# Optimization experiments

Measured on AMD Instinct MI355X. Metric: run time of the kernel, lower is better.

The kernel has to match this reference:

```python
import jax, jax.numpy as jnp
import numpy as np

N = 50000       # nodes
E = 1_600_000   # edges (before self-loops)
IN = 128        # in_channels
OUT = 32        # out_channels per head
H = 2           # heads
NEG_SLOPE = 0.2 # PyG GATConv default leaky-relu slope


def setup_inputs() -> dict:
    key = jax.random.key(0)
    k = jax.random.split(key, 6)
    x = jax.random.normal(k[0], (N, IN), jnp.float32)
    edge_index = jax.random.randint(k[1], (2, E), 0, N, dtype=jnp.int64)
    W = jax.random.normal(k[2], (IN, H * OUT), jnp.float32) / np.sqrt(IN).astype(np.float32)
    att_src = jax.random.normal(k[3], (H, OUT), jnp.float32) * 0.1
    att_dst = jax.random.normal(k[4], (H, OUT), jnp.float32) * 0.1
    bias = jax.random.normal(k[5], (H * OUT,), jnp.float32) * 0.01
    return {"x": x, "edge_index": edge_index, "W": W,
            "att_src": att_src, "att_dst": att_dst, "bias": bias}


def reference(x, edge_index, W, att_src, att_dst, bias):
    n = x.shape[0]
    h_, c = att_src.shape
    # add self-loops (PyG GATConv default add_self_loops=True)
    loops = jnp.arange(n, dtype=edge_index.dtype)
    src = jnp.concatenate([edge_index[0], loops])  # [E+N]
    dst = jnp.concatenate([edge_index[1], loops])  # [E+N]
    # linear transform -> [N, H, C]
    h = (x @ W).reshape(n, h_, c)
    # per-node attention logits per head
    a_src = jnp.einsum('nhc,hc->nh', h, att_src)  # [N, H]
    a_dst = jnp.einsum('nhc,hc->nh', h, att_dst)  # [N, H]
    # per-edge scores
    e = jax.nn.leaky_relu(a_src[src] + a_dst[dst], NEG_SLOPE)  # [E+N, H]
    # segment softmax over incoming edges of each dst node
    seg_max = jax.ops.segment_max(e, dst, num_segments=n)      # [N, H]
    ex = jnp.exp(e - seg_max[dst])
    denom = jax.ops.segment_sum(ex, dst, num_segments=n)       # [N, H]
    alpha = ex / denom[dst]                                    # [E+N, H]
    # weighted scatter-aggregate of source features
    msg = alpha[:, :, None] * h[src]                           # [E+N, H, C]
    out = jax.ops.segment_sum(msg, dst, num_segments=n)        # [N, H, C]
    return out.reshape(n, h_ * c) + bias
```

## Files before the change

kernel.cpp:

```cpp
#include <hip/hip_runtime.h>
#include <hip/hip_fp16.h>

#define N_NODES 50000
#define N_EDGES 1600000
#define IN_CH   128
#define NEG     0.2f
#define NBUK    391
#define BCAP    4608
#define CAP     80
#define CHUNK   4096
#define P_BLOCKS 391
#define PT      512

static __device__ __forceinline__ __half2 u2h2(unsigned u) {
    union { unsigned u; __half2 h; } x; x.u = u; return x.h;
}

__global__ __launch_bounds__(256) void gemm_logits(
    const float* __restrict__ x, const float* __restrict__ W,
    const float* __restrict__ att_src, const float* __restrict__ att_dst,
    unsigned int* __restrict__ hI, float* __restrict__ as_, float* __restrict__ ad_,
    int* __restrict__ gcur)
{
    if (blockIdx.x == 0) {
        for (int i = threadIdx.x; i < NBUK; i += 256) gcur[i] = 0;
    }

    __shared__ float Wl[IN_CH * 64];
    for (int i = threadIdx.x; i < IN_CH * 64; i += 256) Wl[i] = W[i];
    __syncthreads();

    int gid = blockIdx.x * 256 + threadIdx.x;
    int row = gid >> 2;
    int sub = gid & 3;
    if (row >= N_NODES) return;

    float acc[16];
#pragma unroll
    for (int c = 0; c < 16; ++c) acc[c] = 0.f;

    const float* xr = x + (size_t)row * IN_CH;
    for (int k = 0; k < IN_CH; k += 4) {
        float4 xv = *(const float4*)(xr + k);
        float xs[4] = {xv.x, xv.y, xv.z, xv.w};
#pragma unroll
        for (int kk = 0; kk < 4; ++kk) {
            const float* wr = &Wl[(k + kk) * 64 + sub * 16];
#pragma unroll
            for (int c = 0; c < 16; c += 4) {
                float4 wv = *(const float4*)(wr + c);
                acc[c]     += xs[kk] * wv.x;
                acc[c + 1] += xs[kk] * wv.y;
                acc[c + 2] += xs[kk] * wv.z;
                acc[c + 3] += xs[kk] * wv.w;
            }
        }
    }

    float part[16];
#pragma unroll
    for (int i = 0; i < 16; ++i) part[i] = __shfl_xor(acc[i], 2);

    if (sub < 2) {
        union { unsigned int u[16]; uint4 v4[4]; } pk;
#pragma unroll
        for (int i = 0; i < 16; ++i) {
            pk.u[i] = (unsigned)__half_as_ushort(__float2half_rn(acc[i])) |
                      ((unsigned)__half_as_ushort(__float2half_rn(part[i])) << 16);
        }
        uint4* hp = (uint4*)(hI + (size_t)row * 32 + sub * 16);
#pragma unroll
        for (int i = 0; i < 4; ++i) hp[i] = pk.v4[i];
    }

    float s = 0.f, d = 0.f;
#pragma unroll
    for (int c = 0; c < 16; ++c) {
        s += acc[c] * att_src[sub * 16 + c];
        d += acc[c] * att_dst[sub * 16 + c];
    }
    s += __shfl_xor(s, 1);
    d += __shfl_xor(d, 1);
    if ((sub & 1) == 0) {
        as_[row * 2 + (sub >> 1)] = s;
        ad_[row * 2 + (sub >> 1)] = d;
    }
}

__global__ __launch_bounds__(PT) void partition(
    const int* __restrict__ ei, int* __restrict__ gcur,
    unsigned int* __restrict__ barr)
{
    __shared__ int hist[NBUK];
    __shared__ int start[NBUK];
    __shared__ int gbase[NBUK];
    __shared__ int lofs[NBUK];
    __shared__ int wsum[8];
    __shared__ int woff[8];
    __shared__ unsigned int buf[CHUNK];

    int tid = threadIdx.x;
    int lane = tid & 63, wid = tid >> 6;
    int cbase = blockIdx.x * CHUNK;
    int cnt = N_EDGES - cbase;
    if (cnt > CHUNK) cnt = CHUNK;
    int n4 = cnt >> 2;

    for (int i = tid; i < NBUK; i += PT) { hist[i] = 0; lofs[i] = 0; }
    __syncthreads();

    const int4* s4 = (const int4*)ei + (cbase >> 2);
    const int4* d4 = (const int4*)(ei + N_EDGES) + (cbase >> 2);

    int4 dv[2], sv[2];
#pragma unroll
    for (int i = 0; i < 2; ++i) {
        int k = i * PT + tid;
        if (k < n4) {
            dv[i] = d4[k]; sv[i] = s4[k];
            atomicAdd(&hist[dv[i].x >> 7], 1);
            atomicAdd(&hist[dv[i].y >> 7], 1);
            atomicAdd(&hist[dv[i].z >> 7], 1);
            atomicAdd(&hist[dv[i].w >> 7], 1);
        }
    }
    __syncthreads();

    int a = (tid < NBUK) ? hist[tid] : 0;
    int orig = a;
#pragma unroll
    for (int off = 1; off < 64; off <<= 1) {
        int u = __shfl_up(a, off);
        if (lane >= off) a += u;
    }
    if (lane == 63) wsum[wid] = a;
    __syncthreads();
    if (tid == 0) {
        int r = 0;
#pragma unroll
        for (int w = 0; w < 8; ++w) { woff[w] = r; r += wsum[w]; }
    }
    __syncthreads();
    a += woff[wid];
    if (tid < NBUK) {
        start[tid] = a - orig;
        gbase[tid] = atomicAdd(&gcur[tid], orig);
    }
    __syncthreads();

#pragma unroll
    for (int i = 0; i < 2; ++i) {
        int k = i * PT + tid;
        if (k < n4) {
            int dd[4] = {dv[i].x, dv[i].y, dv[i].z, dv[i].w};
            int ss[4] = {sv[i].x, sv[i].y, sv[i].z, sv[i].w};
#pragma unroll
            for (int e = 0; e < 4; ++e) {
                int d = dd[e];
                int bkt = d >> 7;
                int loc = atomicAdd(&lofs[bkt], 1);
                buf[start[bkt] + loc] =
                    (unsigned)ss[e] | ((unsigned)(d & 127) << 16) | ((unsigned)bkt << 23);
            }
        }
    }
    __syncthreads();

    for (int i = tid; i < cnt; i += PT) {
        unsigned u = buf[i];
        int bkt = u >> 23;
        int g = gbase[bkt] + (i - start[bkt]);
        if (g < BCAP) barr[(size_t)bkt * BCAP + g] = u & 0x7FFFFFu;
    }
}

__global__ __launch_bounds__(512) void aggregate(
    const unsigned int* __restrict__ hI, const float* __restrict__ as_,
    const float* __restrict__ ad_, const int* __restrict__ gcur,
    const unsigned int* __restrict__ barr, const float* __restrict__ bias,
    float* __restrict__ out)
{
    __shared__ unsigned short lcol[32 * CAP];
    __shared__ int hist[32];

    int b     = blockIdx.x >> 2;
    int jbase = (blockIdx.x & 3) << 5;
    int tid   = threadIdx.x;
    if (tid < 32) hist[tid] = 0;
    __syncthreads();

    int cnt = gcur[b];
    if (cnt > BCAP) cnt = BCAP;
    const unsigned int* bb = barr + (size_t)b * BCAP;

    for (int i = tid; i < cnt; i += 512) {
        unsigned u = bb[i];
        int r = ((int)(u >> 16) & 127) - jbase;
        if ((unsigned)r < 32u) {
            int k = atomicAdd(&hist[r], 1);
            if (k < CAP) lcol[r * CAP + k] = (unsigned short)(u & 0xFFFFu);
        }
    }
    __syncthreads();

    int lane = tid & 63;
    int wave = tid >> 6;
    int c    = lane & 31;
    int hv   = lane >> 5;
    int sl   = lane & 32;
    float bi0 = bias[c], bi1 = bias[32 + c];

    for (int pass = 0; pass < 2; ++pass) {
        int r = pass * 16 + (wave << 1) + hv;
        int node = b * 128 + jbase + r;
        bool valid = (node < N_NODES);

        float2 adv = valid ? *(const float2*)(ad_ + node * 2) : make_float2(0.f, 0.f);
        float2 asv = valid ? *(const float2*)(as_ + node * 2) : make_float2(0.f, 0.f);

        float t0 = asv.x + adv.x, t1 = asv.y + adv.y;
        float e0 = (t0 > 0.f) ? t0 : NEG * t0;
        float e1 = (t1 > 0.f) ? t1 : NEG * t1;
        float p0s = __expf(e0), p1s = __expf(e1);
        unsigned hs = valid ? hI[(unsigned)node * 32u + c] : 0u;
        __half2 hsh = u2h2(hs);
        float self0 = p0s * __half2float(__low2half(hsh));
        float self1 = p1s * __half2float(__high2half(hsh));
        float s0 = 0.f, s1 = 0.f;

        __half2 z = __float2half2_rn(0.f);
        __half2 acA = z, acB = z, acC = z, acD = z;

        int n = valid ? min(hist[r], CAP) : 0;
        const unsigned short* cb = &lcol[r * CAP];
        int nmax = max(n, __shfl_xor(n, 32));

        for (int base = 0; base < nmax; base += 32) {
            unsigned msrc = 0, packP = 0;
            int myidx = base + c;
            if (myidx < n) {
                int srci = (int)cb[myidx];
                float2 av = *(const float2*)(as_ + srci * 2);
                float u0 = av.x + adv.x, u1 = av.y + adv.y;
                float f0 = (u0 > 0.f) ? u0 : NEG * u0;
                float f1 = (u1 > 0.f) ? u1 : NEG * u1;
                float q0 = __expf(f0), q1 = __expf(f1);
                s0 += q0; s1 += q1;
                msrc  = (unsigned)srci;
                packP = (unsigned)__half_as_ushort(__float2half_rn(q0)) |
                        ((unsigned)__half_as_ushort(__float2half_rn(q1)) << 16);
            }
            int c32 = nmax - base;
            if (c32 > 32) c32 = 32;

            int jj = 0;
            for (; jj + 8 <= c32; jj += 8) {
                unsigned sA = __shfl(msrc, sl + jj);
                unsigned sB = __shfl(msrc, sl + jj + 1);
                unsigned sC = __shfl(msrc, sl + jj + 2);
                unsigned sD = __shfl(msrc, sl + jj + 3);
                unsigned sE = __shfl(msrc, sl + jj + 4);
                unsigned sF = __shfl(msrc, sl + jj + 5);
                unsigned sG = __shfl(msrc, sl + jj + 6);
                unsigned sH = __shfl(msrc, sl + jj + 7);
                unsigned pA = __shfl(packP, sl + jj);
                unsigned pB = __shfl(packP, sl + jj + 1);
                unsigned pC = __shfl(packP, sl + jj + 2);
                unsigned pD = __shfl(packP, sl + jj + 3);
                unsigned pE = __shfl(packP, sl + jj + 4);
                unsigned pF = __shfl(packP, sl + jj + 5);
                unsigned pG = __shfl(packP, sl + jj + 6);
                unsigned pH = __shfl(packP, sl + jj + 7);
                unsigned vA = hI[sA * 32u + c];
                unsigned vB = hI[sB * 32u + c];
                unsigned vC = hI[sC * 32u + c];
                unsigned vD = hI[sD * 32u + c];
                unsigned vE = hI[sE * 32u + c];
                unsigned vF = hI[sF * 32u + c];
                unsigned vG = hI[sG * 32u + c];
                unsigned vH = hI[sH * 32u + c];
                acA = __hfma2(u2h2(vA), u2h2(pA), acA);
                acB = __hfma2(u2h2(vB), u2h2(pB), acB);
                acC = __hfma2(u2h2(vC), u2h2(pC), acC);
                acD = __hfma2(u2h2(vD), u2h2(pD), acD);
                acA = __hfma2(u2h2(vE), u2h2(pE), acA);
                acB = __hfma2(u2h2(vF), u2h2(pF), acB);
                acC = __hfma2(u2h2(vG), u2h2(pG), acC);
                acD = __hfma2(u2h2(vH), u2h2(pH), acD);
            }
            for (; jj < c32; ++jj) {
                unsigned sA = __shfl(msrc, sl + jj);
                unsigned pA = __shfl(packP, sl + jj);
                unsigned vA = hI[sA * 32u + c];
                acA = __hfma2(u2h2(vA), u2h2(pA), acA);
            }
        }

        float2 fA = __half22float2(acA);
        float2 fB = __half22float2(acB);
        float2 fC = __half22float2(acC);
        float2 fD = __half22float2(acD);
        float acc0 = (fA.x + fB.x) + (fC.x + fD.x) + self0;
        float acc1 = (fA.y + fB.y) + (fC.y + fD.y) + self1;

        s0 += __shfl_xor(s0, 16); s1 += __shfl_xor(s1, 16);
        s0 += __shfl_xor(s0, 8);  s1 += __shfl_xor(s1, 8);
        s0 += __shfl_xor(s0, 4);  s1 += __shfl_xor(s1, 4);
        s0 += __shfl_xor(s0, 2);  s1 += __shfl_xor(s1, 2);
        s0 += __shfl_xor(s0, 1);  s1 += __shfl_xor(s1, 1);
        s0 += p0s; s1 += p1s;

        if (valid) {
            out[(size_t)node * 64 + c]      = acc0 / s0 + bi0;
            out[(size_t)node * 64 + 32 + c] = acc1 / s1 + bi1;
        }
    }
}

extern "C" void kernel_launch(void* const* d_in, const int* in_sizes, int n_in,
                              void* d_out, int out_size, void* d_ws, size_t ws_size,
                              hipStream_t stream)
{
    const float* x       = (const float*)d_in[0];
    const int*   ei      = (const int*)d_in[1];
    const float* W       = (const float*)d_in[2];
    const float* att_src = (const float*)d_in[3];
    const float* att_dst = (const float*)d_in[4];
    const float* bias    = (const float*)d_in[5];
    float* out = (float*)d_out;

    char* ws = (char*)d_ws;
    size_t off = 0;
    auto alloc = [&](size_t bytes) -> void* {
        void* p = ws + off;
        off = (off + bytes + 511) & ~(size_t)511;
        return p;
    };
    unsigned int* hI  = (unsigned int*)alloc((size_t)N_NODES * 32 * 4);
    float*  as_ = (float*)alloc((size_t)N_NODES * 2 * 4);
    float*  ad_ = (float*)alloc((size_t)N_NODES * 2 * 4);
    int*    gcur = (int*)alloc((size_t)NBUK * 4);
    unsigned int* barr = (unsigned int*)alloc((size_t)NBUK * BCAP * 4);

    gemm_logits<<<(N_NODES * 4 + 255) / 256, 256, 0, stream>>>(
        x, W, att_src, att_dst, hI, as_, ad_, gcur);
    partition<<<P_BLOCKS, PT, 0, stream>>>(ei, gcur, barr);
    aggregate<<<NBUK * 4, 512, 0, stream>>>(hI, as_, ad_, gcur, barr, bias, out);
}
```

Before: 81.45 us.

## Fuse GEMM and edge partition into one launch; batch 64 edges per aggregate iteration

The node-feature GEMM and the edge bucketing are merged into one kernel whose block ranges split between the two independent jobs. They now run concurrently and share a union of shared memory. Zeroing of the bucket counters moves to a tiny separate kernel. The aggregate loop now loads two 32-edge groups of source indices and logits up front before gathering, to expose more memory-level parallelism. The cost is an extra tiny launch, larger shared memory per block (which may limit occupancy), and more registers in the aggregate loop.

```diff
diff --git a/kernel.cpp b/kernel.cpp
--- a/kernel.cpp
+++ b/kernel.cpp
@@ -10,167 +10,167 @@
 #define CAP     80
 #define CHUNK   4096
 #define P_BLOCKS 391
-#define PT      512
+#define G_BLOCKS 391
 
 static __device__ __forceinline__ __half2 u2h2(unsigned u) {
     union { unsigned u; __half2 h; } x; x.u = u; return x.h;
 }
 
-__global__ __launch_bounds__(256) void gemm_logits(
+__global__ void zero_gcur(int* __restrict__ gcur)
+{
+    if (threadIdx.x < NBUK) gcur[threadIdx.x] = 0;
+}
+
+__global__ __launch_bounds__(512, 6) void fused_gp(
+    const int* __restrict__ ei, int* __restrict__ gcur,
+    unsigned int* __restrict__ barr,
     const float* __restrict__ x, const float* __restrict__ W,
     const float* __restrict__ att_src, const float* __restrict__ att_dst,
-    unsigned int* __restrict__ hI, float* __restrict__ as_, float* __restrict__ ad_,
-    int* __restrict__ gcur)
+    unsigned int* __restrict__ hI, float* __restrict__ as_, float* __restrict__ ad_)
 {
-    if (blockIdx.x == 0) {
-        for (int i = threadIdx.x; i < NBUK; i += 256) gcur[i] = 0;
-    }
-
-    __shared__ float Wl[IN_CH * 64];
-    for (int i = threadIdx.x; i < IN_CH * 64; i += 256) Wl[i] = W[i];
-    __syncthreads();
-
-    int gid = blockIdx.x * 256 + threadIdx.x;
-    int row = gid >> 2;
-    int sub = gid & 3;
-    if (row >= N_NODES) return;
-
-    float acc[16];
-#pragma unroll
-    for (int c = 0; c < 16; ++c) acc[c] = 0.f;
-
-    const float* xr = x + (size_t)row * IN_CH;
-    for (int k = 0; k < IN_CH; k += 4) {
-        float4 xv = *(const float4*)(xr + k);
-        float xs[4] = {xv.x, xv.y, xv.z, xv.w};
-#pragma unroll
-        for (int kk = 0; kk < 4; ++kk) {
-            const float* wr = &Wl[(k + kk) * 64 + sub * 16];
-#pragma unroll
-            for (int c = 0; c < 16; c += 4) {
-                float4 wv = *(const float4*)(wr + c);
-                acc[c]     += xs[kk] * wv.x;
-                acc[c + 1] += xs[kk] * wv.y;
-                acc[c + 2] += xs[kk] * wv.z;
-                acc[c + 3] += xs[kk] * wv.w;
-            }
-        }
-    }
-
-    float part[16];
-#pragma unroll
-    for (int i = 0; i < 16; ++i) part[i] = __shfl_xor(acc[i], 2);
-
-    if (sub < 2) {
-        union { unsigned int u[16]; uint4 v4[4]; } pk;
-#pragma unroll
-        for (int i = 0; i < 16; ++i) {
-            pk.u[i] = (unsigned)__half_as_ushort(__float2half_rn(acc[i])) |
-                      ((unsigned)__half_as_ushort(__float2half_rn(part[i])) << 16);
-        }
-        uint4* hp = (uint4*)(hI + (size_t)row * 32 + sub * 16);
-#pragma unroll
-        for (int i = 0; i < 4; ++i) hp[i] = pk.v4[i];
-    }
-
-    float s = 0.f, d = 0.f;
-#pragma unroll
-    for (int c = 0; c < 16; ++c) {
-        s += acc[c] * att_src[sub * 16 + c];
-        d += acc[c] * att_dst[sub * 16 + c];
-    }
-    s += __shfl_xor(s, 1);
-    d += __shfl_xor(d, 1);
-    if ((sub & 1) == 0) {
-        as_[row * 2 + (sub >> 1)] = s;
-        ad_[row * 2 + (sub >> 1)] = d;
-    }
-}
-
-__global__ __launch_bounds__(PT) void partition(
-    const int* __restrict__ ei, int* __restrict__ gcur,
-    unsigned int* __restrict__ barr)
-{
-    __shared__ int hist[NBUK];
-    __shared__ int start[NBUK];
-    __shared__ int gbase[NBUK];
-    __shared__ int lofs[NBUK];
-    __shared__ int wsum[8];
-    __shared__ int woff[8];
-    __shared__ unsigned int buf[CHUNK];
+    __shared__ union {
+        struct {
+            int hist[NBUK], start[NBUK], gbase[NBUK], lofs[NBUK];
+            int wsum[8], woff[8];
+            unsigned int buf[CHUNK];
+        } p;
+        float w[IN_CH * 64];
+    } sm;
 
     int tid = threadIdx.x;
-    int lane = tid & 63, wid = tid >> 6;
-    int cbase = blockIdx.x * CHUNK;
-    int cnt = N_EDGES - cbase;
-    if (cnt > CHUNK) cnt = CHUNK;
-    int n4 = cnt >> 2;
-
-    for (int i = tid; i < NBUK; i += PT) { hist[i] = 0; lofs[i] = 0; }
-    __syncthreads();
-
-    const int4* s4 = (const int4*)ei + (cbase >> 2);
-    const int4* d4 = (const int4*)(ei + N_EDGES) + (cbase >> 2);
-
-    int4 dv[2], sv[2];
-#pragma unroll
-    for (int i = 0; i < 2; ++i) {
-        int k = i * PT + tid;
-        if (k < n4) {
-            dv[i] = d4[k]; sv[i] = s4[k];
-            atomicAdd(&hist[dv[i].x >> 7], 1);
-            atomicAdd(&hist[dv[i].y >> 7], 1);
-            atomicAdd(&hist[dv[i].z >> 7], 1);
-            atomicAdd(&hist[dv[i].w >> 7], 1);
-        }
-    }
-    __syncthreads();
-
-    int a = (tid < NBUK) ? hist[tid] : 0;
-    int orig = a;
-#pragma unroll
-    for (int off = 1; off < 64; off <<= 1) {
-        int u = __shfl_up(a, off);
-        if (lane >= off) a += u;
-    }
-    if (lane == 63) wsum[wid] = a;
-    __syncthreads();
-    if (tid == 0) {
-        int r = 0;
-#pragma unroll
-        for (int w = 0; w < 8; ++w) { woff[w] = r; r += wsum[w]; }
-    }
-    __syncthreads();
-    a += woff[wid];
-    if (tid < NBUK) {
-        start[tid] = a - orig;
-        gbase[tid] = atomicAdd(&gcur[tid], orig);
-    }
-    __syncthreads();
-
-#pragma unroll
-    for (int i = 0; i < 2; ++i) {
-        int k = i * PT + tid;
-        if (k < n4) {
-            int dd[4] = {dv[i].x, dv[i].y, dv[i].z, dv[i].w};
-            int ss[4] = {sv[i].x, sv[i].y, sv[i].z, sv[i].w};
-#pragma unroll
-            for (int e = 0; e < 4; ++e) {
-                int d = dd[e];
-                int bkt = d >> 7;
-                int loc = atomicAdd(&lofs[bkt], 1);
-                buf[start[bkt] + loc] =
-                    (unsigned)ss[e] | ((unsigned)(d & 127) << 16) | ((unsigned)bkt << 23);
-            }
-        }
-    }
-    __syncthreads();
-
-    for (int i = tid; i < cnt; i += PT) {
-        unsigned u = buf[i];
-        int bkt = u >> 23;
-        int g = gbase[bkt] + (i - start[bkt]);
-        if (g < BCAP) barr[(size_t)bkt * BCAP + g] = u & 0x7FFFFFu;
+
+    if (blockIdx.x < P_BLOCKS) {
+        int lane = tid & 63, wid = tid >> 6;
+        int cbase = blockIdx.x * CHUNK;
+        int cnt = N_EDGES - cbase;
+        if (cnt > CHUNK) cnt = CHUNK;
+        int n4 = cnt >> 2;
+
+        for (int i = tid; i < NBUK; i += 512) { sm.p.hist[i] = 0; sm.p.lofs[i] = 0; }
+        __syncthreads();
+
+        const int4* s4 = (const int4*)ei + (cbase >> 2);
+        const int4* d4 = (const int4*)(ei + N_EDGES) + (cbase >> 2);
+
+        int4 dv[2], sv[2];
+#pragma unroll
+        for (int i = 0; i < 2; ++i) {
+            int k = i * 512 + tid;
+            if (k < n4) {
+                dv[i] = d4[k]; sv[i] = s4[k];
+                atomicAdd(&sm.p.hist[dv[i].x >> 7], 1);
+                atomicAdd(&sm.p.hist[dv[i].y >> 7], 1);
+                atomicAdd(&sm.p.hist[dv[i].z >> 7], 1);
+                atomicAdd(&sm.p.hist[dv[i].w >> 7], 1);
+            }
+        }
+        __syncthreads();
+
+        int a = (tid < NBUK) ? sm.p.hist[tid] : 0;
+        int orig = a;
+#pragma unroll
+        for (int off = 1; off < 64; off <<= 1) {
+            int u = __shfl_up(a, off);
+            if (lane >= off) a += u;
+        }
+        if (lane == 63) sm.p.wsum[wid] = a;
+        __syncthreads();
+        if (tid == 0) {
+            int r = 0;
+#pragma unroll
+            for (int w = 0; w < 8; ++w) { sm.p.woff[w] = r; r += sm.p.wsum[w]; }
+        }
+        __syncthreads();
+        a += sm.p.woff[wid];
+        if (tid < NBUK) {
+            sm.p.start[tid] = a - orig;
+            sm.p.gbase[tid] = atomicAdd(&gcur[tid], orig);
+        }
+        __syncthreads();
+
+#pragma unroll
+        for (int i = 0; i < 2; ++i) {
+            int k = i * 512 + tid;
+            if (k < n4) {
+                int dd[4] = {dv[i].x, dv[i].y, dv[i].z, dv[i].w};
+                int ss[4] = {sv[i].x, sv[i].y, sv[i].z, sv[i].w};
+#pragma unroll
+                for (int e = 0; e < 4; ++e) {
+                    int d = dd[e];
+                    int bkt = d >> 7;
+                    int loc = atomicAdd(&sm.p.lofs[bkt], 1);
+                    sm.p.buf[sm.p.start[bkt] + loc] =
+                        (unsigned)ss[e] | ((unsigned)(d & 127) << 16) | ((unsigned)bkt << 23);
+                }
+            }
+        }
+        __syncthreads();
+
+        for (int i = tid; i < cnt; i += 512) {
+            unsigned u = sm.p.buf[i];
+            int bkt = u >> 23;
+            int g = sm.p.gbase[bkt] + (i - sm.p.start[bkt]);
+            if (g < BCAP) barr[(size_t)bkt * BCAP + g] = u & 0x7FFFFFu;
+        }
+    } else {
+        for (int i = tid; i < IN_CH * 64; i += 512) sm.w[i] = W[i];
+        __syncthreads();
+
+        int gid = (blockIdx.x - P_BLOCKS) * 512 + tid;
+        int row = gid >> 2;
+        int sub = gid & 3;
+        if (row >= N_NODES) return;
+
+        float acc[16];
+#pragma unroll
+        for (int c = 0; c < 16; ++c) acc[c] = 0.f;
+
+        const float* xr = x + (size_t)row * IN_CH;
+        for (int k = 0; k < IN_CH; k += 4) {
+            float4 xv = *(const float4*)(xr + k);
+            float xs[4] = {xv.x, xv.y, xv.z, xv.w};
+#pragma unroll
+            for (int kk = 0; kk < 4; ++kk) {
+                const float* wr = &sm.w[(k + kk) * 64 + sub * 16];
+#pragma unroll
+                for (int c = 0; c < 16; c += 4) {
+                    float4 wv = *(const float4*)(wr + c);
+                    acc[c]     += xs[kk] * wv.x;
+                    acc[c + 1] += xs[kk] * wv.y;
+                    acc[c + 2] += xs[kk] * wv.z;
+                    acc[c + 3] += xs[kk] * wv.w;
+                }
+            }
+        }
+
+        float part[16];
+#pragma unroll
+        for (int i = 0; i < 16; ++i) part[i] = __shfl_xor(acc[i], 2);
+
+        if (sub < 2) {
+            union { unsigned int u[16]; uint4 v4[4]; } pk;
+#pragma unroll
+            for (int i = 0; i < 16; ++i) {
+                pk.u[i] = (unsigned)__half_as_ushort(__float2half_rn(acc[i])) |
+                          ((unsigned)__half_as_ushort(__float2half_rn(part[i])) << 16);
+            }
+            uint4* hp = (uint4*)(hI + (size_t)row * 32 + sub * 16);
+#pragma unroll
+            for (int i = 0; i < 4; ++i) hp[i] = pk.v4[i];
+        }
+
+        float s = 0.f, d = 0.f;
+#pragma unroll
+        for (int c = 0; c < 16; ++c) {
+            s += acc[c] * att_src[sub * 16 + c];
+            d += acc[c] * att_dst[sub * 16 + c];
+        }
+        s += __shfl_xor(s, 1);
+        d += __shfl_xor(d, 1);
+        if ((sub & 1) == 0) {
+            as_[row * 2 + (sub >> 1)] = s;
+            ad_[row * 2 + (sub >> 1)] = d;
+        }
     }
 }
 
@@ -235,42 +235,56 @@
         const unsigned short* cb = &lcol[r * CAP];
         int nmax = max(n, __shfl_xor(n, 32));
 
-        for (int base = 0; base < nmax; base += 32) {
-            unsigned msrc = 0, packP = 0;
-            int myidx = base + c;
-            if (myidx < n) {
-                int srci = (int)cb[myidx];
-                float2 av = *(const float2*)(as_ + srci * 2);
-                float u0 = av.x + adv.x, u1 = av.y + adv.y;
+        for (int base = 0; base < nmax; base += 64) {
+            unsigned ms0 = 0, pp0 = 0, ms1 = 0, pp1 = 0;
+            int i0 = base + c, i1 = base + 32 + c;
+            int sA_ = (i0 < n) ? (int)cb[i0] : -1;
+            int sB_ = (i1 < n) ? (int)cb[i1] : -1;
+            float2 avA = (sA_ >= 0) ? *(const float2*)(as_ + sA_ * 2) : make_float2(0.f, 0.f);
+            float2 avB = (sB_ >= 0) ? *(const float2*)(as_ + sB_ * 2) : make_float2(0.f, 0.f);
+            if (sA_ >= 0) {
+                float u0 = avA.x + adv.x, u1 = avA.y + adv.y;
                 float f0 = (u0 > 0.f) ? u0 : NEG * u0;
                 float f1 = (u1 > 0.f) ? u1 : NEG * u1;
                 float q0 = __expf(f0), q1 = __expf(f1);
                 s0 += q0; s1 += q1;
-                msrc  = (unsigned)srci;
-                packP = (unsigned)__half_as_ushort(__float2half_rn(q0)) |
-                        ((unsigned)__half_as_ushort(__float2half_rn(q1)) << 16);
-            }
-            int c32 = nmax - base;
-            if (c32 > 32) c32 = 32;
+                ms0 = (unsigned)sA_;
+                pp0 = (unsigned)__half_as_ushort(__float2half_rn(q0)) |
+                      ((unsigned)__half_as_ushort(__float2half_rn(q1)) << 16);
+            }
+            if (sB_ >= 0) {
+                float u0 = avB.x + adv.x, u1 = avB.y + adv.y;
+                float f0 = (u0 > 0.f) ? u0 : NEG * u0;
+                float f1 = (u1 > 0.f) ? u1 : NEG * u1;
+                float q0 = __expf(f0), q1 = __expf(f1);
+                s0 += q0; s1 += q1;
+                ms1 = (unsigned)sB_;
+                pp1 = (unsigned)__half_as_ushort(__float2half_rn(q0)) |
+                      ((unsigned)__half_as_ushort(__float2half_rn(q1)) << 16);
+            }
+
+            int rem = nmax - base;
+            int cA = rem < 32 ? rem : 32;
+            int cB = rem - 32; if (cB < 0) cB = 0; else if (cB > 32) cB = 32;
 
             int jj = 0;
-            for (; jj + 8 <= c32; jj += 8) {
-                unsigned sA = __shfl(msrc, sl + jj);
-                unsigned sB = __shfl(msrc, sl + jj + 1);
-                unsigned sC = __shfl(msrc, sl + jj + 2);
-                unsigned sD = __shfl(msrc, sl + jj + 3);
-                unsigned sE = __shfl(msrc, sl + jj + 4);
-                unsigned sF = __shfl(msrc, sl + jj + 5);
-                unsigned sG = __shfl(msrc, sl + jj + 6);
-                unsigned sH = __shfl(msrc, sl + jj + 7);
-                unsigned pA = __shfl(packP, sl + jj);
-                unsigned pB = __shfl(packP, sl + jj + 1);
-                unsigned pC = __shfl(packP, sl + jj + 2);
-                unsigned pD = __shfl(packP, sl + jj + 3);
-                unsigned pE = __shfl(packP, sl + jj + 4);
-                unsigned pF = __shfl(packP, sl + jj + 5);
-                unsigned pG = __shfl(packP, sl + jj + 6);
-                unsigned pH = __shfl(packP, sl + jj + 7);
+            for (; jj + 8 <= cA; jj += 8) {
+                unsigned sA = __shfl(ms0, sl + jj);
+                unsigned sB = __shfl(ms0, sl + jj + 1);
+                unsigned sC = __shfl(ms0, sl + jj + 2);
+                unsigned sD = __shfl(ms0, sl + jj + 3);
+                unsigned sE = __shfl(ms0, sl + jj + 4);
+                unsigned sF = __shfl(ms0, sl + jj + 5);
+                unsigned sG = __shfl(ms0, sl + jj + 6);
+                unsigned sH = __shfl(ms0, sl + jj + 7);
+                unsigned pA = __shfl(pp0, sl + jj);
+                unsigned pB = __shfl(pp0, sl + jj + 1);
+                unsigned pC = __shfl(pp0, sl + jj + 2);
+                unsigned pD = __shfl(pp0, sl + jj + 3);
+                unsigned pE = __shfl(pp0, sl + jj + 4);
+                unsigned pF = __shfl(pp0, sl + jj + 5);
+                unsigned pG = __shfl(pp0, sl + jj + 6);
+                unsigned pH = __shfl(pp0, sl + jj + 7);
                 unsigned vA = hI[sA * 32u + c];
                 unsigned vB = hI[sB * 32u + c];
                 unsigned vC = hI[sC * 32u + c];
@@ -288,9 +302,50 @@
                 acC = __hfma2(u2h2(vG), u2h2(pG), acC);
                 acD = __hfma2(u2h2(vH), u2h2(pH), acD);
             }
-            for (; jj < c32; ++jj) {
-                unsigned sA = __shfl(msrc, sl + jj);
-                unsigned pA = __shfl(packP, sl + jj);
+            for (; jj < cA; ++jj) {
+                unsigned sA = __shfl(ms0, sl + jj);
+                unsigned pA = __shfl(pp0, sl + jj);
+                unsigned vA = hI[sA * 32u + c];
+                acA = __hfma2(u2h2(vA), u2h2(pA), acA);
+            }
+            jj = 0;
+            for (; jj + 8 <= cB; jj += 8) {
+                unsigned sA = __shfl(ms1, sl + jj);
+                unsigned sB = __shfl(ms1, sl + jj + 1);
+                unsigned sC = __shfl(ms1, sl + jj + 2);
+                unsigned sD = __shfl(ms1, sl + jj + 3);
+                unsigned sE = __shfl(ms1, sl + jj + 4);
+                unsigned sF = __shfl(ms1, sl + jj + 5);
+                unsigned sG = __shfl(ms1, sl + jj + 6);
+                unsigned sH = __shfl(ms1, sl + jj + 7);
+                unsigned pA = __shfl(pp1, sl + jj);
+                unsigned pB = __shfl(pp1, sl + jj + 1);
+                unsigned pC = __shfl(pp1, sl + jj + 2);
+                unsigned pD = __shfl(pp1, sl + jj + 3);
+                unsigned pE = __shfl(pp1, sl + jj + 4);
+                unsigned pF = __shfl(pp1, sl + jj + 5);
+                unsigned pG = __shfl(pp1, sl + jj + 6);
+                unsigned pH = __shfl(pp1, sl + jj + 7);
+                unsigned vA = hI[sA * 32u + c];
+                unsigned vB = hI[sB * 32u + c];
+                unsigned vC = hI[sC * 32u + c];
+                unsigned vD = hI[sD * 32u + c];
+                unsigned vE = hI[sE * 32u + c];
+                unsigned vF = hI[sF * 32u + c];
+                unsigned vG = hI[sG * 32u + c];
+                unsigned vH = hI[sH * 32u + c];
+                acA = __hfma2(u2h2(vA), u2h2(pA), acA);
+                acB = __hfma2(u2h2(vB), u2h2(pB), acB);
+                acC = __hfma2(u2h2(vC), u2h2(pC), acC);
+                acD = __hfma2(u2h2(vD), u2h2(pD), acD);
+                acA = __hfma2(u2h2(vE), u2h2(pE), acA);
+                acB = __hfma2(u2h2(vF), u2h2(pF), acB);
+                acC = __hfma2(u2h2(vG), u2h2(pG), acC);
+                acD = __hfma2(u2h2(vH), u2h2(pH), acD);
+            }
+            for (; jj < cB; ++jj) {
+                unsigned sA = __shfl(ms1, sl + jj);
+                unsigned pA = __shfl(pp1, sl + jj);
                 unsigned vA = hI[sA * 32u + c];
                 acA = __hfma2(u2h2(vA), u2h2(pA), acA);
             }
@@ -342,8 +397,8 @@
     int*    gcur = (int*)alloc((size_t)NBUK * 4);
     unsigned int* barr = (unsigned int*)alloc((size_t)NBUK * BCAP * 4);
 
-    gemm_logits<<<(N_NODES * 4 + 255) / 256, 256, 0, stream>>>(
-        x, W, att_src, att_dst, hI, as_, ad_, gcur);
-    partition<<<P_BLOCKS, PT, 0, stream>>>(ei, gcur, barr);
+    zero_gcur<<<1, 512, 0, stream>>>(gcur);
+    fused_gp<<<P_BLOCKS + G_BLOCKS, 512, 0, stream>>>(
+        ei, gcur, barr, x, W, att_src, att_dst, hI, as_, ad_);
     aggregate<<<NBUK * 4, 512, 0, stream>>>(hI, as_, ad_, gcur, barr, bias, out);
 }
```

Measured after the change: 80.88 us. No clear change (-0.7%).

## Precompute edge attention weights during bucket scan and store in LDS

Applied to the files above, without the earlier changes.

Moves the per-edge leaky-relu/exp computation from the aggregation loop into the bucket-scan phase. Each weight is stored as a packed half2 in a new LDS array next to the column index, and the softmax denominators are accumulated with shared-memory float atomics. The gather loop then reads indices and weights from LDS with vector loads instead of using wave shuffles. In exchange, LDS use per block rises by about 10KB, which may lower occupancy, and the LDS float atomics add contention. The scan phase also now does a global as_ gather for every edge in the bucket that belongs to this block.

```diff
diff --git a/kernel.cpp b/kernel.cpp
--- a/kernel.cpp
+++ b/kernel.cpp
@@ -181,12 +181,21 @@
     float* __restrict__ out)
 {
     __shared__ unsigned short lcol[32 * CAP];
-    __shared__ int hist[32];
+    __shared__ unsigned int   lq[32 * CAP];
+    __shared__ float2 advl[32];
+    __shared__ float  sden[64];
+    __shared__ int    hist[32];
 
     int b     = blockIdx.x >> 2;
     int jbase = (blockIdx.x & 3) << 5;
     int tid   = threadIdx.x;
-    if (tid < 32) hist[tid] = 0;
+    if (tid < 32) {
+        hist[tid] = 0;
+        int node = b * 128 + jbase + tid;
+        advl[tid] = (node < N_NODES) ? *(const float2*)(ad_ + node * 2)
+                                     : make_float2(0.f, 0.f);
+    }
+    if (tid < 64) sden[tid] = 0.f;
     __syncthreads();
 
     int cnt = gcur[b];
@@ -197,8 +206,22 @@
         unsigned u = bb[i];
         int r = ((int)(u >> 16) & 127) - jbase;
         if ((unsigned)r < 32u) {
+            int srci = (int)(u & 0xFFFFu);
+            float2 adv = advl[r];
+            float2 av  = *(const float2*)(as_ + srci * 2);
+            float u0 = av.x + adv.x, u1 = av.y + adv.y;
+            float f0 = (u0 > 0.f) ? u0 : NEG * u0;
+            float f1 = (u1 > 0.f) ? u1 : NEG * u1;
+            float q0 = __expf(f0), q1 = __expf(f1);
             int k = atomicAdd(&hist[r], 1);
-            if (k < CAP) lcol[r * CAP + k] = (unsigned short)(u & 0xFFFFu);
+            if (k < CAP) {
+                atomicAdd(&sden[r * 2],     q0);
+                atomicAdd(&sden[r * 2 + 1], q1);
+                lcol[r * CAP + k] = (unsigned short)srci;
+                lq[r * CAP + k] =
+                    (unsigned)__half_as_ushort(__float2half_rn(q0)) |
+                    ((unsigned)__half_as_ushort(__float2half_rn(q1)) << 16);
+            }
         }
     }
     __syncthreads();
@@ -207,7 +230,6 @@
     int wave = tid >> 6;
     int c    = lane & 31;
     int hv   = lane >> 5;
-    int sl   = lane & 32;
     float bi0 = bias[c], bi1 = bias[32 + c];
 
     for (int pass = 0; pass < 2; ++pass) {
@@ -215,7 +237,7 @@
         int node = b * 128 + jbase + r;
         bool valid = (node < N_NODES);
 
-        float2 adv = valid ? *(const float2*)(ad_ + node * 2) : make_float2(0.f, 0.f);
+        float2 adv = advl[r];
         float2 asv = valid ? *(const float2*)(as_ + node * 2) : make_float2(0.f, 0.f);
 
         float t0 = asv.x + adv.x, t1 = asv.y + adv.y;
@@ -226,74 +248,41 @@
         __half2 hsh = u2h2(hs);
         float self0 = p0s * __half2float(__low2half(hsh));
         float self1 = p1s * __half2float(__high2half(hsh));
-        float s0 = 0.f, s1 = 0.f;
 
         __half2 z = __float2half2_rn(0.f);
         __half2 acA = z, acB = z, acC = z, acD = z;
 
         int n = valid ? min(hist[r], CAP) : 0;
-        const unsigned short* cb = &lcol[r * CAP];
-        int nmax = max(n, __shfl_xor(n, 32));
-
-        for (int base = 0; base < nmax; base += 32) {
-            unsigned msrc = 0, packP = 0;
-            int myidx = base + c;
-            if (myidx < n) {
-                int srci = (int)cb[myidx];
-                float2 av = *(const float2*)(as_ + srci * 2);
-                float u0 = av.x + adv.x, u1 = av.y + adv.y;
-                float f0 = (u0 > 0.f) ? u0 : NEG * u0;
-                float f1 = (u1 > 0.f) ? u1 : NEG * u1;
-                float q0 = __expf(f0), q1 = __expf(f1);
-                s0 += q0; s1 += q1;
-                msrc  = (unsigned)srci;
-                packP = (unsigned)__half_as_ushort(__float2half_rn(q0)) |
-                        ((unsigned)__half_as_ushort(__float2half_rn(q1)) << 16);
-            }
-            int c32 = nmax - base;
-            if (c32 > 32) c32 = 32;
-
-            int jj = 0;
-            for (; jj + 8 <= c32; jj += 8) {
-                unsigned sA = __shfl(msrc, sl + jj);
-                unsigned sB = __shfl(msrc, sl + jj + 1);
-                unsigned sC = __shfl(msrc, sl + jj + 2);
-                unsigned sD = __shfl(msrc, sl + jj + 3);
-                unsigned sE = __shfl(msrc, sl + jj + 4);
-                unsigned sF = __shfl(msrc, sl + jj + 5);
-                unsigned sG = __shfl(msrc, sl + jj + 6);
-                unsigned sH = __shfl(msrc, sl + jj + 7);
-                unsigned pA = __shfl(packP, sl + jj);
-                unsigned pB = __shfl(packP, sl + jj + 1);
-                unsigned pC = __shfl(packP, sl + jj + 2);
-                unsigned pD = __shfl(packP, sl + jj + 3);
-                unsigned pE = __shfl(packP, sl + jj + 4);
-                unsigned pF = __shfl(packP, sl + jj + 5);
-                unsigned pG = __shfl(packP, sl + jj + 6);
-                unsigned pH = __shfl(packP, sl + jj + 7);
-                unsigned vA = hI[sA * 32u + c];
-                unsigned vB = hI[sB * 32u + c];
-                unsigned vC = hI[sC * 32u + c];
-                unsigned vD = hI[sD * 32u + c];
-                unsigned vE = hI[sE * 32u + c];
-                unsigned vF = hI[sF * 32u + c];
-                unsigned vG = hI[sG * 32u + c];
-                unsigned vH = hI[sH * 32u + c];
-                acA = __hfma2(u2h2(vA), u2h2(pA), acA);
-                acB = __hfma2(u2h2(vB), u2h2(pB), acB);
-                acC = __hfma2(u2h2(vC), u2h2(pC), acC);
-                acD = __hfma2(u2h2(vD), u2h2(pD), acD);
-                acA = __hfma2(u2h2(vE), u2h2(pE), acA);
-                acB = __hfma2(u2h2(vF), u2h2(pF), acB);
-                acC = __hfma2(u2h2(vG), u2h2(pG), acC);
-                acD = __hfma2(u2h2(vH), u2h2(pH), acD);
-            }
-            for (; jj < c32; ++jj) {
-                unsigned sA = __shfl(msrc, sl + jj);
-                unsigned pA = __shfl(packP, sl + jj);
-                unsigned vA = hI[sA * 32u + c];
-                acA = __hfma2(u2h2(vA), u2h2(pA), acA);
-            }
+        int bo = r * CAP;
+
+        int j = 0;
+        for (; j + 8 <= n; j += 8) {
+            ushort4 c0 = *(const ushort4*)&lcol[bo + j];
+            ushort4 c1 = *(const ushort4*)&lcol[bo + j + 4];
+            uint4   q0 = *(const uint4*)&lq[bo + j];
+            uint4   q1 = *(const uint4*)&lq[bo + j + 4];
+            unsigned vA = hI[(unsigned)c0.x * 32u + c];
+            unsigned vB = hI[(unsigned)c0.y * 32u + c];
+            unsigned vC = hI[(unsigned)c0.z * 32u + c];
+            unsigned vD = hI[(unsigned)c0.w * 32u + c];
+            unsigned vE = hI[(unsigned)c1.x * 32u + c];
+            unsigned vF = hI[(unsigned)c1.y * 32u + c];
+            unsigned vG = hI[(unsigned)c1.z * 32u + c];
+            unsigned vH = hI[(unsigned)c1.w * 32u + c];
+            acA = __hfma2(u2h2(vA), u2h2(q0.x), acA);
+            acB = __hfma2(u2h2(vB), u2h2(q0.y), acB);
+            acC = __hfma2(u2h2(vC), u2h2(q0.z), acC);
+            acD = __hfma2(u2h2(vD), u2h2(q0.w), acD);
+            acA = __hfma2(u2h2(vE), u2h2(q1.x), acA);
+            acB = __hfma2(u2h2(vF), u2h2(q1.y), acB);
+            acC = __hfma2(u2h2(vG), u2h2(q1.z), acC);
+            acD = __hfma2(u2h2(vH), u2h2(q1.w), acD);
+        }
+        for (; j < n; ++j) {
+            unsigned srci = lcol[bo + j];
+            unsigned qp   = lq[bo + j];
+            unsigned vA = hI[srci * 32u + c];
+            acA = __hfma2(u2h2(vA), u2h2(qp), acA);
         }
 
         float2 fA = __half22float2(acA);
@@ -303,12 +292,8 @@
         float acc0 = (fA.x + fB.x) + (fC.x + fD.x) + self0;
         float acc1 = (fA.y + fB.y) + (fC.y + fD.y) + self1;
 
-        s0 += __shfl_xor(s0, 16); s1 += __shfl_xor(s1, 16);
-        s0 += __shfl_xor(s0, 8);  s1 += __shfl_xor(s1, 8);
-        s0 += __shfl_xor(s0, 4);  s1 += __shfl_xor(s1, 4);
-        s0 += __shfl_xor(s0, 2);  s1 += __shfl_xor(s1, 2);
-        s0 += __shfl_xor(s0, 1);  s1 += __shfl_xor(s1, 1);
-        s0 += p0s; s1 += p1s;
+        float s0 = sden[r * 2]     + p0s;
+        float s1 = sden[r * 2 + 1] + p1s;
 
         if (valid) {
             out[(size_t)node * 64 + c]      = acc0 / s0 + bi0;
```

Measured after the change: 86.92 us. 6.7% more time.

## Replace partition histogram+scan with fixed-capacity per-bucket LDS slots and overflow atomics

Applied to the files above, without the earlier changes.

The partition kernel drops its two-pass histogram, prefix-scan and compaction in favour of one pass. Each edge is appended into a fixed 32-entry LDS slot per bucket, and any overflow goes straight to global memory through a global atomic. CHUNK is halved and the block count doubled, so each thread handles one int4 and per-bucket counts stay near the LDS capacity. This removes several barriers and the scan, but the write-out loop now scans all 391x32 slots, mostly empty ones, and global atomics go up.

```diff
diff --git a/kernel.cpp b/kernel.cpp
--- a/kernel.cpp
+++ b/kernel.cpp
@@ -8,9 +8,10 @@
 #define NBUK    391
 #define BCAP    4608
 #define CAP     80
-#define CHUNK   4096
-#define P_BLOCKS 391
+#define CHUNK   2048
+#define P_BLOCKS 782
 #define PT      512
+#define LCAP    32
 
 static __device__ __forceinline__ __half2 u2h2(unsigned u) {
     union { unsigned u; __half2 h; } x; x.u = u; return x.h;
@@ -91,86 +92,61 @@
     const int* __restrict__ ei, int* __restrict__ gcur,
     unsigned int* __restrict__ barr)
 {
-    __shared__ int hist[NBUK];
-    __shared__ int start[NBUK];
+    __shared__ unsigned int buf[NBUK * LCAP];
+    __shared__ int lofs[NBUK];
     __shared__ int gbase[NBUK];
-    __shared__ int lofs[NBUK];
-    __shared__ int wsum[8];
-    __shared__ int woff[8];
-    __shared__ unsigned int buf[CHUNK];
 
     int tid = threadIdx.x;
-    int lane = tid & 63, wid = tid >> 6;
     int cbase = blockIdx.x * CHUNK;
     int cnt = N_EDGES - cbase;
     if (cnt > CHUNK) cnt = CHUNK;
     int n4 = cnt >> 2;
 
-    for (int i = tid; i < NBUK; i += PT) { hist[i] = 0; lofs[i] = 0; }
+    for (int i = tid; i < NBUK; i += PT) lofs[i] = 0;
     __syncthreads();
 
     const int4* s4 = (const int4*)ei + (cbase >> 2);
     const int4* d4 = (const int4*)(ei + N_EDGES) + (cbase >> 2);
 
-    int4 dv[2], sv[2];
-#pragma unroll
-    for (int i = 0; i < 2; ++i) {
-        int k = i * PT + tid;
-        if (k < n4) {
-            dv[i] = d4[k]; sv[i] = s4[k];
-            atomicAdd(&hist[dv[i].x >> 7], 1);
-            atomicAdd(&hist[dv[i].y >> 7], 1);
-            atomicAdd(&hist[dv[i].z >> 7], 1);
-            atomicAdd(&hist[dv[i].w >> 7], 1);
-        }
-    }
-    __syncthreads();
-
-    int a = (tid < NBUK) ? hist[tid] : 0;
-    int orig = a;
-#pragma unroll
-    for (int off = 1; off < 64; off <<= 1) {
-        int u = __shfl_up(a, off);
-        if (lane >= off) a += u;
-    }
-    if (lane == 63) wsum[wid] = a;
-    __syncthreads();
-    if (tid == 0) {
-        int r = 0;
-#pragma unroll
-        for (int w = 0; w < 8; ++w) { woff[w] = r; r += wsum[w]; }
-    }
-    __syncthreads();
-    a += woff[wid];
+    if (tid < n4) {
+        int4 dv = d4[tid];
+        int4 sv = s4[tid];
+        int dd[4] = {dv.x, dv.y, dv.z, dv.w};
+        int ss[4] = {sv.x, sv.y, sv.z, sv.w};
+#pragma unroll
+        for (int e = 0; e < 4; ++e) {
+            int d = dd[e];
+            int bkt = d >> 7;
+            unsigned w = (unsigned)ss[e] | ((unsigned)(d & 127) << 16) |
+                         ((unsigned)bkt << 23);
+            int loc = atomicAdd(&lofs[bkt], 1);
+            if (loc < LCAP) {
+                buf[(bkt << 5) + loc] = w;
+            } else {
+                int g = atomicAdd(&gcur[bkt], 1);
+                if (g < BCAP) barr[(size_t)bkt * BCAP + g] = w & 0x7FFFFFu;
+            }
+        }
+    }
+    __syncthreads();
+
     if (tid < NBUK) {
-        start[tid] = a - orig;
-        gbase[tid] = atomicAdd(&gcur[tid], orig);
-    }
-    __syncthreads();
-
-#pragma unroll
-    for (int i = 0; i < 2; ++i) {
-        int k = i * PT + tid;
-        if (k < n4) {
-            int dd[4] = {dv[i].x, dv[i].y, dv[i].z, dv[i].w};
-            int ss[4] = {sv[i].x, sv[i].y, sv[i].z, sv[i].w};
-#pragma unroll
-            for (int e = 0; e < 4; ++e) {
-                int d = dd[e];
-                int bkt = d >> 7;
-                int loc = atomicAdd(&lofs[bkt], 1);
-                buf[start[bkt] + loc] =
-                    (unsigned)ss[e] | ((unsigned)(d & 127) << 16) | ((unsigned)bkt << 23);
-            }
-        }
-    }
-    __syncthreads();
-
-    for (int i = tid; i < cnt; i += PT) {
-        unsigned u = buf[i];
-        int bkt = u >> 23;
-        int g = gbase[bkt] + (i - start[bkt]);
-        if (g < BCAP) barr[(size_t)bkt * BCAP + g] = u & 0x7FFFFFu;
+        int c = lofs[tid];
+        if (c > LCAP) c = LCAP;
+        gbase[tid] = (c > 0) ? atomicAdd(&gcur[tid], c) : 0;
+    }
+    __syncthreads();
+
+    for (int i = tid; i < NBUK * LCAP; i += PT) {
+        int bkt  = i >> 5;
+        int slot = i & (LCAP - 1);
+        int c = lofs[bkt];
+        if (c > LCAP) c = LCAP;
+        if (slot < c) {
+            int g = gbase[bkt] + slot;
+            if (g < BCAP)
+                barr[(size_t)bkt * BCAP + g] = buf[i] & 0x7FFFFFu;
+        }
     }
 }
 
```

New measurement: 92.84 us. 1.14x slower.
